# Kernel optimization log

Measured on AMD Instinct MI355X. Metric: run time of the kernel, lower is better.

Reference implementation:

```python
import jax, jax.numpy as jnp
import numpy as np

L, S, N, E, H = 2048, 2048, 4, 512, 8
D = E // H


def _rel_shift(x):
    # Faithful replication of the torch code's _rel_shift (which keeps [:1],
    # collapsing the S axis to size 1): x is (L, N, H, S) -> (L, N, H, 1).
    l, n, h, s = x.shape
    pad = jnp.concatenate([x, jnp.zeros((l, n, h, 1), x.dtype)], axis=-1)  # L,N,H,S+1
    p = jnp.transpose(pad, (0, 3, 1, 2))  # L,S+1,N,H  ('lnhs->lsnh')
    # view([S+1, L, N, H])[:1] == first L*N*H flat elements reshaped to (1,L,N,H)
    p = p.reshape(-1)[: l * n * h].reshape(1, l, n, h)
    return jnp.transpose(p, (1, 2, 3, 0))  # 'slnh->lnhs' -> (L,N,H,1)


def setup_inputs() -> dict:
    key = jax.random.key(0)
    ks = jax.random.split(key, 9)
    sc_in = (2.0 / (E + 3 * E)) ** 0.5  # xavier-ish scale
    sc_sq = (1.0 / E) ** 0.5
    return {
        "query": jax.random.normal(ks[0], (L, N, E), jnp.float32),
        "key": jax.random.normal(ks[1], (S, N, E), jnp.float32),
        "value": jax.random.normal(ks[2], (S, N, E), jnp.float32),
        "sin_pos_enc": jax.random.normal(ks[3], (S, E), jnp.float32),
        "in_proj_weight": jax.random.normal(ks[4], (3 * E, E), jnp.float32) * sc_in,
        "in_proj_bias": jnp.zeros((3 * E,), jnp.float32),
        "out_w": jax.random.normal(ks[5], (E, E), jnp.float32) * sc_sq,
        "out_b": jnp.zeros((E,), jnp.float32),
        "rel_proj_w": jax.random.normal(ks[6], (E, E), jnp.float32) * sc_sq,
        "rel_u": jax.random.normal(ks[7], (H, D), jnp.float32) * 0.1,
        "rel_v": jax.random.normal(ks[8], (H, D), jnp.float32) * 0.1,
    }


def reference(query, key, value, sin_pos_enc, in_proj_weight, in_proj_bias,
              out_w, out_b, rel_proj_w, rel_u, rel_v):
    def src_proj(x, base):
        w = in_proj_weight[base * E:(base + 1) * E]
        b = in_proj_bias[base * E:(base + 1) * E]
        y = x @ w.T + b  # T,N,E
        return y.reshape(y.shape[0], -1, H, D)  # T,N,H,D

    q = src_proj(query, 0)   # L,N,H,D
    k = src_proj(key, 1)     # S,N,H,D
    v = src_proj(value, 2)   # S,N,H,D
    rel_pos = (sin_pos_enc @ rel_proj_w.T).reshape(S, H, D)  # S,H,D

    term_ac = jnp.einsum('lnhd,snhd->lnhs', q + rel_u, k)      # L,N,H,S
    term_bd = jnp.einsum('lnhd,shd->lnhs', q + rel_v, rel_pos) # L,N,H,S
    term_bd = _rel_shift(term_bd)                              # L,N,H,1

    att = jax.nn.softmax((term_ac + term_bd) / (D ** 0.5), axis=-1)  # L,N,H,S
    out = jnp.einsum('lnhs,snhd->lnhd', att, v).reshape(L, -1, E)    # L,N,E
    out = out @ out_w.T + out_b
    att_weights = jnp.transpose(att.mean(axis=-2), (1, 0, 2))  # N,L,S
    return (out, att_weights)
```

## Files before the change

kernel.cpp:

```cpp
#include <hip/hip_runtime.h>
#include <hip/hip_bf16.h>
#include <stdint.h>


#define L_Q 2048
#define S_K 2048
#define N_B 4
#define E_D 512
#define H_N 8
#define D_H 64

typedef unsigned short u16;
typedef short v8s __attribute__((ext_vector_type(8)));
typedef float v4f __attribute__((ext_vector_type(4)));

#define MFMA16(a, b, c) __builtin_amdgcn_mfma_f32_16x16x32_bf16(a, b, c, 0, 0, 0)

__device__ __forceinline__ float bf2f(u16 u) {
  unsigned int x = ((unsigned int)u) << 16;
  return __builtin_bit_cast(float, x);
}
__device__ __forceinline__ u16 f2bf(float f) {
  unsigned int x = __builtin_bit_cast(unsigned int, f);
  x += 0x7FFFu + ((x >> 16) & 1u);
  return (u16)(x >> 16);
}
__device__ __forceinline__ float expc(float x) {
  return __expf(fminf(fmaxf(x, -30.f), 30.f));
}

struct Cvt8 {
  const float* s[8];
  u16* d[8];
};
__global__ __launch_bounds__(256) void cvt_k(Cvt8 a) {
  const size_t t = ((size_t)blockIdx.x * 256 + threadIdx.x) * 4;
  const size_t cum[9] = {0,        4194304,  8388608,  12582912, 13369344,
                         13631488, 13633024, 13633536, 13634048};
  if (t >= cum[8]) return;
  int sg = 0;
#pragma unroll
  for (int i = 1; i < 8; i++) sg += (t >= cum[i]);
  const size_t off = t - cum[sg];
  const v4f x = *(const v4f*)(a.s[sg] + off);
  ushort4 o;
  o.x = f2bf(x[0]);
  o.y = f2bf(x[1]);
  o.z = f2bf(x[2]);
  o.w = f2bf(x[3]);
  *(ushort4*)(a.d[sg] + off) = o;
}

__device__ __forceinline__ void gemm_core(const u16* A, const u16* W, int m0,
                                          int n0, u16* As, u16* Bs,
                                          v4f acc[4][4]) {
  const int lane = threadIdx.x & 63;
  const int w = threadIdx.x >> 6;
  const int wr = w >> 1, wc = w & 1;
  const int q = lane >> 4, c = lane & 15;
#pragma unroll
  for (int i = 0; i < 4; i++)
#pragma unroll
    for (int j = 0; j < 4; j++) acc[i][j] = (v4f){0.f, 0.f, 0.f, 0.f};
  for (int kk = 0; kk < 16; ++kk) {
    const u16* ga = A + (size_t)(m0 + lane) * E_D + kk * 32 + w * 8;
    const u16* gb = W + (size_t)(n0 + lane) * E_D + kk * 32 + w * 8;
    const v8s va0 = *(const v8s*)ga;
    const v8s va1 = *(const v8s*)(ga + 64 * E_D);
    const v8s vb0 = *(const v8s*)gb;
    const v8s vb1 = *(const v8s*)(gb + 64 * E_D);
    __syncthreads();
    *(v8s*)(As + w * 1032 + lane * 8) = va0;
    *(v8s*)(As + w * 1032 + 512 + lane * 8) = va1;
    *(v8s*)(Bs + w * 1032 + lane * 8) = vb0;
    *(v8s*)(Bs + w * 1032 + 512 + lane * 8) = vb1;
    __syncthreads();
    v8s a[4], b[4];
#pragma unroll
    for (int i = 0; i < 4; i++)
      a[i] = *(const v8s*)(As + q * 1032 + (wr * 64 + i * 16 + c) * 8);
#pragma unroll
    for (int j = 0; j < 4; j++)
      b[j] = *(const v8s*)(Bs + q * 1032 + (wc * 64 + j * 16 + c) * 8);
#pragma unroll
    for (int i = 0; i < 4; i++)
#pragma unroll
      for (int j = 0; j < 4; j++) acc[i][j] = MFMA16(a[i], b[j], acc[i][j]);
  }
}

__global__ __launch_bounds__(256) void gemm_qkv(
    const u16* __restrict__ qb, const u16* __restrict__ kb,
    const u16* __restrict__ vb, const u16* __restrict__ Wallb,
    const u16* __restrict__ biasb, const u16* __restrict__ rel_ub,
    u16* __restrict__ Qw, u16* __restrict__ Kw, u16* __restrict__ Vt) {
  __shared__ __align__(16) u16 As[4 * 1032];
  __shared__ __align__(16) u16 Bs[4 * 1032];
  const int z = blockIdx.z;
  const u16* A = (z == 0) ? qb : ((z == 1) ? kb : vb);
  const int m0 = blockIdx.x * 128, n0 = blockIdx.y * 128;
  v4f acc[4][4];
  gemm_core(A, Wallb + (size_t)z * E_D * E_D, m0, n0, As, Bs, acc);
  const int lane = threadIdx.x & 63, w = threadIdx.x >> 6;
  const int wr = w >> 1, wc = w & 1;
  const int q = lane >> 4, c = lane & 15;
#pragma unroll
  for (int j = 0; j < 4; j++) {
    const int jg = n0 + wc * 64 + j * 16 + c;
    const int h = jg >> 6, d = jg & 63;
    float add =
        bf2f(biasb[z * E_D + jg]) + ((z == 0) ? bf2f(rel_ub[jg]) : 0.f);
#pragma unroll
    for (int i = 0; i < 4; i++) {
#pragma unroll
      for (int r = 0; r < 4; r++) {
        const int mg = m0 + wr * 64 + i * 16 + q * 4 + r;
        const int row = mg >> 2, nn = mg & 3;
        const u16 o = f2bf(acc[i][j][r] + add);
        if (z == 0)
          Qw[((size_t)(nn * H_N + h) * L_Q + row) * D_H + d] = o;
        else if (z == 1)
          Kw[((size_t)(nn * H_N + h) * S_K + row) * D_H + d] = o;
        else
          Vt[((size_t)(nn * H_N + h) * D_H + d) * S_K + row] = o;
      }
    }
  }
}

__global__ __launch_bounds__(256) void gemm_out(const u16* __restrict__ Actx,
                                                const u16* __restrict__ Woutb,
                                                const u16* __restrict__ boutb,
                                                float* __restrict__ out) {
  __shared__ __align__(16) u16 As[4 * 1032];
  __shared__ __align__(16) u16 Bs[4 * 1032];
  const int m0 = blockIdx.x * 128, n0 = blockIdx.y * 128;
  v4f acc[4][4];
  gemm_core(Actx, Woutb, m0, n0, As, Bs, acc);
  const int lane = threadIdx.x & 63, w = threadIdx.x >> 6;
  const int wr = w >> 1, wc = w & 1;
  const int q = lane >> 4, c = lane & 15;
#pragma unroll
  for (int j = 0; j < 4; j++) {
    const int jg = n0 + wc * 64 + j * 16 + c;
    const float bb = bf2f(boutb[jg]);
#pragma unroll
    for (int i = 0; i < 4; i++) {
#pragma unroll
      for (int r = 0; r < 4; r++) {
        const int mg = m0 + wr * 64 + i * 16 + q * 4 + r;
        out[(size_t)mg * E_D + jg] = acc[i][j][r] + bb;
      }
    }
  }
}

__global__ __launch_bounds__(256) void flash_pv(
    const u16* __restrict__ Qw, const u16* __restrict__ Kw,
    const u16* __restrict__ Vt, u16* __restrict__ Actx,
    float* __restrict__ Rbuf) {
  __shared__ __align__(16) u16 Qs[8 * 520];
  __shared__ __align__(16) u16 Ks[8 * 520];
  __shared__ __align__(16) u16 Vs[8 * 520];
  __shared__ __align__(16) short Ps[4 * 8 * 16 * 8];
  const int lane = threadIdx.x & 63, w = threadIdx.x >> 6;
  const int q = lane >> 4, c = lane & 15;
  const int l0 = blockIdx.x * 64;
  const int nh = blockIdx.z * H_N + blockIdx.y;
  {
    const u16* g = Qw + ((size_t)nh * L_Q + l0 + lane) * D_H + w * 8;
    const v8s vq0 = *(const v8s*)g;
    const v8s vq1 = *(const v8s*)(g + 32);
    *(v8s*)(Qs + w * 520 + lane * 8) = vq0;
    *(v8s*)(Qs + (w + 4) * 520 + lane * 8) = vq1;
  }
  v4f ctx[4];
  float s_run[4];
#pragma unroll
  for (int i = 0; i < 4; i++) {
    ctx[i] = (v4f){0.f, 0.f, 0.f, 0.f};
    s_run[i] = 0.f;
  }
  __syncthreads();
  const v8s aq0 = *(const v8s*)(Qs + q * 520 + (w * 16 + c) * 8);
  const v8s aq1 = *(const v8s*)(Qs + (q + 4) * 520 + (w * 16 + c) * 8);
  short* pw = Ps + w * (8 * 16 * 8);
  for (int s0 = 0; s0 < S_K; s0 += 64) {
    const u16* gk = Kw + ((size_t)nh * S_K + s0 + lane) * D_H + w * 8;
    const u16* gv = Vt + ((size_t)nh * D_H + lane) * S_K + s0 + w * 8;
    const v8s vk0 = *(const v8s*)gk;
    const v8s vk1 = *(const v8s*)(gk + 32);
    const v8s vv0 = *(const v8s*)gv;
    const v8s vv1 = *(const v8s*)(gv + 32);
    __syncthreads();
    *(v8s*)(Ks + w * 520 + lane * 8) = vk0;
    *(v8s*)(Ks + (w + 4) * 520 + lane * 8) = vk1;
    *(v8s*)(Vs + w * 520 + lane * 8) = vv0;
    *(v8s*)(Vs + (w + 4) * 520 + lane * 8) = vv1;
    __syncthreads();
    v4f sv[4];
#pragma unroll
    for (int jt = 0; jt < 4; jt++) {
      const v8s bk0 = *(const v8s*)(Ks + q * 520 + (jt * 16 + c) * 8);
      const v8s bk1 = *(const v8s*)(Ks + (q + 4) * 520 + (jt * 16 + c) * 8);
      v4f zz = (v4f){0.f, 0.f, 0.f, 0.f};
      zz = MFMA16(aq0, bk0, zz);
      zz = MFMA16(aq1, bk1, zz);
      sv[jt] = zz;
    }
#pragma unroll
    for (int r = 0; r < 4; r++) {
      const int row = q * 4 + r;
#pragma unroll
      for (int jt = 0; jt < 4; jt++) {
        const float p = expc(sv[jt][r] * 0.125f);
        s_run[r] += p;
        const int sl = jt * 16 + c;
        pw[((sl >> 3) * 16 + row) * 8 + (sl & 7)] = (short)f2bf(p);
      }
    }
    __threadfence_block();
    const v8s ap0 = *(const v8s*)(pw + (q * 16 + c) * 8);
    const v8s ap1 = *(const v8s*)(pw + ((q + 4) * 16 + c) * 8);
#pragma unroll
    for (int ds = 0; ds < 4; ds++) {
      const v8s bv0 = *(const v8s*)(Vs + q * 520 + (ds * 16 + c) * 8);
      const v8s bv1 = *(const v8s*)(Vs + (q + 4) * 520 + (ds * 16 + c) * 8);
      ctx[ds] = MFMA16(ap0, bv0, ctx[ds]);
      ctx[ds] = MFMA16(ap1, bv1, ctx[ds]);
    }
  }
#pragma unroll
  for (int r = 0; r < 4; r++) {
    float s = s_run[r];
    s += __shfl_xor(s, 1);
    s += __shfl_xor(s, 2);
    s += __shfl_xor(s, 4);
    s += __shfl_xor(s, 8);
    s_run[r] = s;
  }
#pragma unroll
  for (int r = 0; r < 4; r++) {
    const float rr = 1.0f / s_run[r];
    const int l = l0 + w * 16 + q * 4 + r;
#pragma unroll
    for (int ds = 0; ds < 4; ds++) {
      Actx[((size_t)l * N_B + blockIdx.z) * E_D + blockIdx.y * D_H + ds * 16 +
           c] = f2bf(ctx[ds][r] * rr);
    }
    if (c == 0) Rbuf[(size_t)nh * L_Q + l] = rr;
  }
}

__global__ __launch_bounds__(256) void attw_k(const u16* __restrict__ Qw,
                                              const u16* __restrict__ Kw,
                                              const float* __restrict__ Rbuf,
                                              float* __restrict__ AW) {
  __shared__ __align__(16) u16 Qs[8 * 520];
  __shared__ __align__(16) u16 Ks[8 * 520];
  const int lane = threadIdx.x & 63, w = threadIdx.x >> 6;
  const int q = lane >> 4, c = lane & 15;
  const int s_base = blockIdx.x * 256;
  const int l0 = blockIdx.y * 64;
  const int n = blockIdx.z;
  v4f aw[4][4];
#pragma unroll
  for (int ss = 0; ss < 4; ss++)
#pragma unroll
    for (int jt = 0; jt < 4; jt++) aw[ss][jt] = (v4f){0.f, 0.f, 0.f, 0.f};
  for (int h = 0; h < H_N; ++h) {
    const int nh = n * H_N + h;
    float rr[4];
#pragma unroll
    for (int r = 0; r < 4; r++)
      rr[r] = Rbuf[(size_t)nh * L_Q + l0 + w * 16 + q * 4 + r];
    v8s aq0, aq1;
    for (int ss = 0; ss < 4; ++ss) {
      const u16* gk =
          Kw + ((size_t)nh * S_K + s_base + ss * 64 + lane) * D_H + w * 8;
      const v8s vk0 = *(const v8s*)gk;
      const v8s vk1 = *(const v8s*)(gk + 32);
      v8s vq0, vq1;
      if (ss == 0) {
        const u16* g = Qw + ((size_t)nh * L_Q + l0 + lane) * D_H + w * 8;
        vq0 = *(const v8s*)g;
        vq1 = *(const v8s*)(g + 32);
      }
      __syncthreads();
      if (ss == 0) {
        *(v8s*)(Qs + w * 520 + lane * 8) = vq0;
        *(v8s*)(Qs + (w + 4) * 520 + lane * 8) = vq1;
      }
      *(v8s*)(Ks + w * 520 + lane * 8) = vk0;
      *(v8s*)(Ks + (w + 4) * 520 + lane * 8) = vk1;
      __syncthreads();
      if (ss == 0) {
        aq0 = *(const v8s*)(Qs + q * 520 + (w * 16 + c) * 8);
        aq1 = *(const v8s*)(Qs + (q + 4) * 520 + (w * 16 + c) * 8);
      }
#pragma unroll
      for (int jt = 0; jt < 4; jt++) {
        const v8s bk0 = *(const v8s*)(Ks + q * 520 + (jt * 16 + c) * 8);
        const v8s bk1 = *(const v8s*)(Ks + (q + 4) * 520 + (jt * 16 + c) * 8);
        v4f zz = (v4f){0.f, 0.f, 0.f, 0.f};
        zz = MFMA16(aq0, bk0, zz);
        zz = MFMA16(aq1, bk1, zz);
#pragma unroll
        for (int r = 0; r < 4; r++)
          aw[ss][jt][r] += expc(zz[r] * 0.125f) * rr[r];
      }
    }
  }
#pragma unroll
  for (int ss = 0; ss < 4; ss++)
#pragma unroll
    for (int jt = 0; jt < 4; jt++)
#pragma unroll
      for (int r = 0; r < 4; r++) {
        const int l = l0 + w * 16 + q * 4 + r;
        const int s = s_base + ss * 64 + jt * 16 + c;
        AW[((size_t)n * L_Q + l) * S_K + s] = aw[ss][jt][r] * 0.125f;
      }
}

extern "C" void kernel_launch(void* const* d_in, const int* in_sizes, int n_in,
                              void* d_out, int out_size, void* d_ws,
                              size_t ws_size, hipStream_t stream) {
  char* ws = (char*)d_ws;
  u16* Wallb = (u16*)(ws);
  u16* Woutb = (u16*)(ws + 1572864);
  u16* biasb = (u16*)(ws + 2097152);
  u16* boutb = (u16*)(ws + 2100224);
  u16* rel_ub = (u16*)(ws + 2101248);
  u16* Qw = (u16*)(ws + 4194304);
  u16* Kw = (u16*)(ws + 12582912);
  u16* Vt = (u16*)(ws + 20971520);
  float* Rbuf = (float*)(ws + 29360128);

  float* out = (float*)d_out;
  char* sc = (char*)d_out + 16777216;
  u16* qb = (u16*)(sc);
  u16* kb = (u16*)(sc + 8388608);
  u16* vb = (u16*)(sc + 16777216);
  u16* Actx = (u16*)(sc + 25165824);
  float* AW = out + (size_t)L_Q * N_B * E_D;

  Cvt8 a;
  a.s[0] = (const float*)d_in[0];  a.d[0] = qb;
  a.s[1] = (const float*)d_in[1];  a.d[1] = kb;
  a.s[2] = (const float*)d_in[2];  a.d[2] = vb;
  a.s[3] = (const float*)d_in[4];  a.d[3] = Wallb;
  a.s[4] = (const float*)d_in[6];  a.d[4] = Woutb;
  a.s[5] = (const float*)d_in[5];  a.d[5] = biasb;
  a.s[6] = (const float*)d_in[7];  a.d[6] = boutb;
  a.s[7] = (const float*)d_in[9];  a.d[7] = rel_ub;

  hipLaunchKernelGGL(cvt_k, dim3(13315), dim3(256), 0, stream, a);
  hipLaunchKernelGGL(gemm_qkv, dim3(64, 4, 3), dim3(256), 0, stream, qb, kb,
                     vb, Wallb, biasb, rel_ub, Qw, Kw, Vt);
  hipLaunchKernelGGL(flash_pv, dim3(32, 8, 4), dim3(256), 0, stream, Qw, Kw,
                     Vt, Actx, Rbuf);
  hipLaunchKernelGGL(gemm_out, dim3(64, 4, 1), dim3(256), 0, stream, Actx,
                     Woutb, boutb, out);
  hipLaunchKernelGGL(attw_k, dim3(8, 32, 4), dim3(256), 0, stream, Qw, Kw,
                     Rbuf, AW);
}
```

Baseline: 339.6 us.

## Transpose flash MFMA operands, pack P via cvt_pk, fast exp2, direct LDS loads

```diff
diff --git a/kernel.cpp b/kernel.cpp
--- a/kernel.cpp
+++ b/kernel.cpp
@@ -11,6 +11,7 @@
 #define D_H 64
 
 typedef unsigned short u16;
+typedef unsigned int u32;
 typedef short v8s __attribute__((ext_vector_type(8)));
 typedef float v4f __attribute__((ext_vector_type(4)));
 
@@ -25,9 +26,33 @@
   x += 0x7FFFu + ((x >> 16) & 1u);
   return (u16)(x >> 16);
 }
-__device__ __forceinline__ float expc(float x) {
-  return __expf(fminf(fmaxf(x, -30.f), 30.f));
-}
+
+__device__ __forceinline__ float expfast(float sv) {
+  const float x =
+      __builtin_amdgcn_fmed3f(sv * 0.18033688011112042f, -43.2809f, 43.2809f);
+#if __has_builtin(__builtin_amdgcn_exp2f)
+  return __builtin_amdgcn_exp2f(x);
+#else
+  return __expf(x * 0.6931471805599453f);
+#endif
+}
+
+__device__ __forceinline__ u32 cvtpk(float lo, float hi) {
+  u32 r;
+  asm("v_cvt_pk_bf16_f32 %0, %1, %2" : "=v"(r) : "v"(lo), "v"(hi));
+  return r;
+}
+
+#if __has_builtin(__builtin_amdgcn_global_load_lds)
+#define HAVE_GLDS 1
+__device__ __forceinline__ void glds16(const u16* g, u16* l) {
+  __builtin_amdgcn_global_load_lds(
+      (const __attribute__((address_space(1))) void*)g,
+      (__attribute__((address_space(3))) void*)l, 16, 0, 0);
+}
+#else
+#define HAVE_GLDS 0
+#endif
 
 struct Cvt8 {
   const float* s[8];
@@ -65,6 +90,14 @@
   for (int kk = 0; kk < 16; ++kk) {
     const u16* ga = A + (size_t)(m0 + lane) * E_D + kk * 32 + w * 8;
     const u16* gb = W + (size_t)(n0 + lane) * E_D + kk * 32 + w * 8;
+#if HAVE_GLDS
+    __syncthreads();
+    glds16(ga, As + w * 1032);
+    glds16(ga + 64 * E_D, As + w * 1032 + 512);
+    glds16(gb, Bs + w * 1032);
+    glds16(gb + 64 * E_D, Bs + w * 1032 + 512);
+    __syncthreads();
+#else
     const v8s va0 = *(const v8s*)ga;
     const v8s va1 = *(const v8s*)(ga + 64 * E_D);
     const v8s vb0 = *(const v8s*)gb;
@@ -75,6 +108,7 @@
     *(v8s*)(Bs + w * 1032 + lane * 8) = vb0;
     *(v8s*)(Bs + w * 1032 + 512 + lane * 8) = vb1;
     __syncthreads();
+#endif
     v8s a[4], b[4];
 #pragma unroll
     for (int i = 0; i < 4; i++)
@@ -162,7 +196,7 @@
   __shared__ __align__(16) u16 Qs[8 * 520];
   __shared__ __align__(16) u16 Ks[8 * 520];
   __shared__ __align__(16) u16 Vs[8 * 520];
-  __shared__ __align__(16) short Ps[4 * 8 * 16 * 8];
+  __shared__ __align__(16) u32 PsU[4 * 16 * 36];
   const int lane = threadIdx.x & 63, w = threadIdx.x >> 6;
   const int q = lane >> 4, c = lane & 15;
   const int l0 = blockIdx.x * 64;
@@ -175,16 +209,13 @@
     *(v8s*)(Qs + (w + 4) * 520 + lane * 8) = vq1;
   }
   v4f ctx[4];
-  float s_run[4];
-#pragma unroll
-  for (int i = 0; i < 4; i++) {
-    ctx[i] = (v4f){0.f, 0.f, 0.f, 0.f};
-    s_run[i] = 0.f;
-  }
+#pragma unroll
+  for (int i = 0; i < 4; i++) ctx[i] = (v4f){0.f, 0.f, 0.f, 0.f};
+  float s_run = 0.f;
   __syncthreads();
   const v8s aq0 = *(const v8s*)(Qs + q * 520 + (w * 16 + c) * 8);
   const v8s aq1 = *(const v8s*)(Qs + (q + 4) * 520 + (w * 16 + c) * 8);
-  short* pw = Ps + w * (8 * 16 * 8);
+  u32* pwU = PsU + w * (16 * 36);
   for (int s0 = 0; s0 < S_K; s0 += 64) {
     const u16* gk = Kw + ((size_t)nh * S_K + s0 + lane) * D_H + w * 8;
     const u16* gv = Vt + ((size_t)nh * D_H + lane) * S_K + s0 + w * 8;
@@ -198,58 +229,48 @@
     *(v8s*)(Vs + w * 520 + lane * 8) = vv0;
     *(v8s*)(Vs + (w + 4) * 520 + lane * 8) = vv1;
     __syncthreads();
-    v4f sv[4];
 #pragma unroll
     for (int jt = 0; jt < 4; jt++) {
       const v8s bk0 = *(const v8s*)(Ks + q * 520 + (jt * 16 + c) * 8);
       const v8s bk1 = *(const v8s*)(Ks + (q + 4) * 520 + (jt * 16 + c) * 8);
       v4f zz = (v4f){0.f, 0.f, 0.f, 0.f};
-      zz = MFMA16(aq0, bk0, zz);
-      zz = MFMA16(aq1, bk1, zz);
-      sv[jt] = zz;
-    }
-#pragma unroll
-    for (int r = 0; r < 4; r++) {
-      const int row = q * 4 + r;
-#pragma unroll
-      for (int jt = 0; jt < 4; jt++) {
-        const float p = expc(sv[jt][r] * 0.125f);
-        s_run[r] += p;
-        const int sl = jt * 16 + c;
-        pw[((sl >> 3) * 16 + row) * 8 + (sl & 7)] = (short)f2bf(p);
-      }
+      zz = MFMA16(bk0, aq0, zz);
+      zz = MFMA16(bk1, aq1, zz);
+      const float p0 = expfast(zz[0]);
+      const float p1 = expfast(zz[1]);
+      const float p2 = expfast(zz[2]);
+      const float p3 = expfast(zz[3]);
+      s_run += (p0 + p1) + (p2 + p3);
+      uint2 pk;
+      pk.x = cvtpk(p0, p1);
+      pk.y = cvtpk(p2, p3);
+      *(uint2*)(pwU + c * 36 + jt * 8 + q * 2) = pk;
     }
     __threadfence_block();
-    const v8s ap0 = *(const v8s*)(pw + (q * 16 + c) * 8);
-    const v8s ap1 = *(const v8s*)(pw + ((q + 4) * 16 + c) * 8);
+    const v8s bp0 = *(const v8s*)(pwU + c * 36 + q * 4);
+    const v8s bp1 = *(const v8s*)(pwU + c * 36 + 16 + q * 4);
 #pragma unroll
     for (int ds = 0; ds < 4; ds++) {
-      const v8s bv0 = *(const v8s*)(Vs + q * 520 + (ds * 16 + c) * 8);
-      const v8s bv1 = *(const v8s*)(Vs + (q + 4) * 520 + (ds * 16 + c) * 8);
-      ctx[ds] = MFMA16(ap0, bv0, ctx[ds]);
-      ctx[ds] = MFMA16(ap1, bv1, ctx[ds]);
-    }
-  }
-#pragma unroll
-  for (int r = 0; r < 4; r++) {
-    float s = s_run[r];
-    s += __shfl_xor(s, 1);
-    s += __shfl_xor(s, 2);
-    s += __shfl_xor(s, 4);
-    s += __shfl_xor(s, 8);
-    s_run[r] = s;
-  }
-#pragma unroll
-  for (int r = 0; r < 4; r++) {
-    const float rr = 1.0f / s_run[r];
-    const int l = l0 + w * 16 + q * 4 + r;
-#pragma unroll
-    for (int ds = 0; ds < 4; ds++) {
-      Actx[((size_t)l * N_B + blockIdx.z) * E_D + blockIdx.y * D_H + ds * 16 +
-           c] = f2bf(ctx[ds][r] * rr);
-    }
-    if (c == 0) Rbuf[(size_t)nh * L_Q + l] = rr;
-  }
+      const v8s av0 = *(const v8s*)(Vs + q * 520 + (ds * 16 + c) * 8);
+      const v8s av1 = *(const v8s*)(Vs + (q + 4) * 520 + (ds * 16 + c) * 8);
+      ctx[ds] = MFMA16(av0, bp0, ctx[ds]);
+      ctx[ds] = MFMA16(av1, bp1, ctx[ds]);
+    }
+  }
+  float s = s_run;
+  s += __shfl_xor(s, 16);
+  s += __shfl_xor(s, 32);
+  const float rr = 1.0f / s;
+  const int l = l0 + w * 16 + c;
+#pragma unroll
+  for (int ds = 0; ds < 4; ds++) {
+    uint2 o;
+    o.x = (u32)f2bf(ctx[ds][0] * rr) | ((u32)f2bf(ctx[ds][1] * rr) << 16);
+    o.y = (u32)f2bf(ctx[ds][2] * rr) | ((u32)f2bf(ctx[ds][3] * rr) << 16);
+    *(uint2*)(Actx + ((size_t)l * N_B + blockIdx.z) * E_D + blockIdx.y * D_H +
+              ds * 16 + q * 4) = o;
+  }
+  if (q == 0) Rbuf[(size_t)nh * L_Q + l] = rr;
 }
 
 __global__ __launch_bounds__(256) void attw_k(const u16* __restrict__ Qw,
@@ -307,7 +328,7 @@
         zz = MFMA16(aq1, bk1, zz);
 #pragma unroll
         for (int r = 0; r < 4; r++)
-          aw[ss][jt][r] += expc(zz[r] * 0.125f) * rr[r];
+          aw[ss][jt][r] += expfast(zz[r]) * rr[r];
       }
     }
   }
```

Measured after the change: 314.4 us. 1.08x faster.
